# Kernel tuning notes

Hardware: AMD Instinct MI355X
Metric: run time of the kernel (lower is better)

Reference implementation:

```python
import jax, jax.numpy as jnp
import numpy as np

N, FR, P, B = 8192, 128, 4194304, 64
LH1, LH2 = 128, 64

def _mlp(x, W1, b1, W2, b2, W3, b3):
    h = jnp.tanh(x @ W1 + b1)
    h = jnp.tanh(h @ W2 + b2)
    return h @ W3 + b3  # [N, 1]

def setup_inputs() -> dict:
    key = jax.random.key(0)
    ks = jax.random.split(key, 12)
    r = jax.random.normal(ks[0], (N, FR), jnp.float32)
    xyz = jax.random.uniform(ks[1], (N, 3), jnp.float32) * 60.0  # box so distances >> sigma
    p0 = jax.random.randint(ks[2], (P,), 0, N)
    off = jax.random.randint(ks[3], (P,), 1, N)  # avoid self-pairs (D2=0)
    pairs = jnp.stack([p0, (p0 + off) % N], axis=1).astype(jnp.int32)
    num_pairs = jnp.full((B,), P // B, dtype=jnp.int32)
    def lin(k, fin, fout):
        return (jax.random.normal(k, (fin, fout), jnp.float32) / np.sqrt(fin)).astype(jnp.float32)
    sW1, sW2, sW3 = lin(ks[4], FR, LH1), lin(ks[5], LH1, LH2), lin(ks[6], LH2, 1)
    eW1, eW2, eW3 = lin(ks[7], FR, LH1), lin(ks[8], LH1, LH2), lin(ks[9], LH2, 1)
    z1, z2, z3 = jnp.zeros((LH1,), jnp.float32), jnp.zeros((LH2,), jnp.float32), jnp.zeros((1,), jnp.float32)
    return dict(r=r, xyz=xyz, pairs=pairs, num_pairs=num_pairs,
                sW1=sW1, sb1=z1, sW2=sW2, sb2=z2, sW3=sW3, sb3=z3,
                eW1=eW1, eb1=z1, eW2=eW2, eb2=z2, eW3=eW3, eb3=z3)

def reference(r, xyz, pairs, num_pairs, sW1, sb1, sW2, sb2, sW3, sb3,
              eW1, eb1, eW2, eb2, eW3, eb3):
    # D2 gathered at pairs == squared distance between the two atoms of each pair
    dx = xyz[pairs[:, 1]] - xyz[pairs[:, 0]]          # [P, 3]
    D2 = jnp.sum(dx * dx, axis=1, keepdims=True)       # [P, 1]
    inv_D = D2 ** -0.5
    sigma = 4.0 + 10.0 * _mlp(r, sW1, sb1, sW2, sb2, sW3, sb3) ** 2   # [N, 1]
    epsilon = 0.1 * _mlp(r, eW1, eb1, eW2, eb2, eW3, eb3) ** 2        # [N, 1]
    sigma_mixed = jnp.sqrt(sigma[pairs[:, 0]] * sigma[pairs[:, 1]])    # [P, 1]
    epsilon_mixed = jnp.sqrt(epsilon[pairs[:, 0]] * epsilon[pairs[:, 1]])
    s = sigma_mixed * inv_D
    s6 = s ** 6
    E_pair = 4.0 * epsilon_mixed * (s6 * s6 - s6)       # [P, 1]
    seg = jnp.repeat(jnp.arange(B), num_pairs, total_repeat_length=P)
    E = jax.ops.segment_sum(E_pair, seg, num_segments=B)  # [B, 1]
    return E
```

## Files before the change

kernel.cpp:

```cpp
#include <hip/hip_runtime.h>
#include <hip/hip_fp16.h>

#define NATOM 8192
#define FR    128
#define NSEG  64
#define PB    256
#define PT    1024
#define PPT   16

typedef _Float16 v8h __attribute__((ext_vector_type(8)));
typedef _Float16 v4h __attribute__((ext_vector_type(4)));
typedef float    v4f __attribute__((ext_vector_type(4)));

__device__ __forceinline__ float fast_tanh(float x)
{
    float t = __expf(2.f * x);
    return 1.f - 2.f * __builtin_amdgcn_rcpf(t + 1.f);
}

__global__ __launch_bounds__(512) void k_mm(
    const float* __restrict__ r, const float* __restrict__ xyz,
    const float* __restrict__ w1s, const float* __restrict__ b1s,
    const float* __restrict__ w2s, const float* __restrict__ b2s,
    const float* __restrict__ w3s, const float* __restrict__ b3s,
    const float* __restrict__ w1e, const float* __restrict__ b1e,
    const float* __restrict__ w2e, const float* __restrict__ b2e,
    const float* __restrict__ w3e, const float* __restrict__ b3e,
    float4* __restrict__ atomd)
{
    extern __shared__ char ldsraw[];
    _Float16* Wh  = (_Float16*)ldsraw;
    _Float16* Wl  = Wh + 32768;
    _Float16* h1h = Wh;
    _Float16* h1l = Wh + 16384;
    _Float16* W2h = Wh + 32768;
    _Float16* W2l = Wh + 49152;
    float*    mArr = (float*)(ldsraw + 131072);

    const int tid = threadIdx.x;
    const int a0  = blockIdx.x * 64;
    const int l = tid & 63, wv = tid >> 6;
    const int row16 = l & 15, kgrp = l >> 4;
    const int at = wv & 3, chf = wv >> 2;

#pragma unroll
    for (int i = 0; i < 8; ++i) {
        int g = i * 512 + tid;
        int c = g & 255, ch = g >> 8;
        const float* wp = (c < 128) ? (w1s + c) : (w1e + (c - 128));
        v8h hh, ll;
#pragma unroll
        for (int j = 0; j < 8; ++j) {
            float x = wp[(ch * 8 + j) * 128];
            _Float16 h = (_Float16)x;
            hh[j] = h;
            ll[j] = (_Float16)((x - (float)h) * 4096.f);
        }
        int sw = c * 16 + (ch ^ (c & 15));
        *(v8h*)(Wh + sw * 8) = hh;
        *(v8h*)(Wl + sw * 8) = ll;
    }

    v8h rh[4], rl[4];
    {
        const float* rb = r + (size_t)(a0 + at * 16 + row16) * FR + kgrp * 8;
#pragma unroll
        for (int ks = 0; ks < 4; ++ks) {
            float4 x0 = *(const float4*)(rb + ks * 32);
            float4 x1 = *(const float4*)(rb + ks * 32 + 4);
            float xs[8] = {x0.x, x0.y, x0.z, x0.w, x1.x, x1.y, x1.z, x1.w};
#pragma unroll
            for (int j = 0; j < 8; ++j) {
                _Float16 h = (_Float16)xs[j];
                rh[ks][j] = h;
                rl[ks][j] = (_Float16)((xs[j] - (float)h) * 4096.f);
            }
        }
    }
    __syncthreads();

    v4h hpack[8], lpack[8];
#pragma unroll
    for (int ct = 0; ct < 8; ++ct) {
        int crow = chf * 128 + ct * 16 + row16;
        v4f a = {0.f, 0.f, 0.f, 0.f}, cr = {0.f, 0.f, 0.f, 0.f};
        int rbo = crow * 128, sw = crow & 15;
#pragma unroll
        for (int ks = 0; ks < 4; ++ks) {
            int off = rbo + (((ks * 4 + kgrp) ^ sw) * 8);
            v8h wh = *(const v8h*)(Wh + off);
            v8h wl = *(const v8h*)(Wl + off);
            a  = __builtin_amdgcn_mfma_f32_16x16x32_f16(wh, rh[ks], a,  0, 0, 0);
            cr = __builtin_amdgcn_mfma_f32_16x16x32_f16(wh, rl[ks], cr, 0, 0, 0);
            cr = __builtin_amdgcn_mfma_f32_16x16x32_f16(wl, rh[ks], cr, 0, 0, 0);
        }
        int colb = chf * 128 + ct * 16 + kgrp * 4;
        const float* bp = (colb < 128) ? (b1s + colb) : (b1e + (colb - 128));
        float4 bv = *(const float4*)bp;
        float bvx[4] = {bv.x, bv.y, bv.z, bv.w};
#pragma unroll
        for (int j = 0; j < 4; ++j) {
            float v = fast_tanh(a[j] + cr[j] * 2.44140625e-4f + bvx[j]);
            _Float16 h = (_Float16)v;
            hpack[ct][j] = h;
            lpack[ct][j] = (_Float16)((v - (float)h) * 4096.f);
        }
    }
    __syncthreads();

    {
        int arow = at * 16 + row16;
#pragma unroll
        for (int ct = 0; ct < 8; ++ct) {
            int colb = chf * 128 + ct * 16 + kgrp * 4;
            int chs = (colb >> 3) ^ row16;
            int off = arow * 256 + chs * 8 + (colb & 7);
            *(v4h*)(h1h + off) = hpack[ct];
            *(v4h*)(h1l + off) = lpack[ct];
        }
#pragma unroll
        for (int i = 0; i < 4; ++i) {
            int g = i * 512 + tid;
            int c = g & 127, ch = g >> 7;
            const float* wp = (c < 64) ? (w2s + c) : (w2e + (c - 64));
            v8h hh, ll;
#pragma unroll
            for (int j = 0; j < 8; ++j) {
                float x = wp[(ch * 8 + j) * 64];
                _Float16 h = (_Float16)x;
                hh[j] = h;
                ll[j] = (_Float16)((x - (float)h) * 4096.f);
            }
            int sw = c * 16 + (ch ^ (c & 15));
            *(v8h*)(W2h + sw * 8) = hh;
            *(v8h*)(W2l + sw * 8) = ll;
        }
    }
    __syncthreads();

    {
        const int arow = at * 16 + row16;
        v8h bh[4], bl[4];
#pragma unroll
        for (int ks = 0; ks < 4; ++ks) {
            int chunk = chf * 16 + ks * 4 + kgrp;
            int off = arow * 256 + ((chunk ^ row16) * 8);
            bh[ks] = *(const v8h*)(h1h + off);
            bl[ks] = *(const v8h*)(h1l + off);
        }
        float ps = 0.f;
#pragma unroll
        for (int ct2 = 0; ct2 < 4; ++ct2) {
            int c2 = chf * 64 + ct2 * 16 + row16;
            v4f a = {0.f, 0.f, 0.f, 0.f}, cr = {0.f, 0.f, 0.f, 0.f};
            int rbo = c2 * 128, sw = c2 & 15;
#pragma unroll
            for (int ks = 0; ks < 4; ++ks) {
                int off = rbo + (((ks * 4 + kgrp) ^ sw) * 8);
                v8h wh = *(const v8h*)(W2h + off);
                v8h wl = *(const v8h*)(W2l + off);
                a  = __builtin_amdgcn_mfma_f32_16x16x32_f16(wh, bh[ks], a,  0, 0, 0);
                cr = __builtin_amdgcn_mfma_f32_16x16x32_f16(wh, bl[ks], cr, 0, 0, 0);
                cr = __builtin_amdgcn_mfma_f32_16x16x32_f16(wl, bh[ks], cr, 0, 0, 0);
            }
            int cb = ct2 * 16 + kgrp * 4;
            float4 b2v = *(const float4*)((chf ? b2e : b2s) + cb);
            float4 w3v = *(const float4*)((chf ? w3e : w3s) + cb);
            float b2x[4] = {b2v.x, b2v.y, b2v.z, b2v.w};
            float w3x[4] = {w3v.x, w3v.y, w3v.z, w3v.w};
#pragma unroll
            for (int j = 0; j < 4; ++j) {
                float h2 = fast_tanh(a[j] + cr[j] * 2.44140625e-4f + b2x[j]);
                ps = fmaf(h2, w3x[j], ps);
            }
        }
        ps += __shfl_xor(ps, 16);
        ps += __shfl_xor(ps, 32);
        if (l < 16) mArr[chf * 64 + at * 16 + l] = ps + (chf ? b3e[0] : b3s[0]);
    }
    __syncthreads();

    if (tid < 64) {
        int atom = a0 + tid;
        float ms = mArr[tid], me = mArr[64 + tid];
        float sg = fmaf(10.f * ms, ms, 4.f);
        float p  = sg * sqrtf(sg);
        float q  = 0.31622776601683794f * fabsf(me);
        __half2 pq = __halves2half2(__float2half(p), __float2half(q));
        atomd[atom] = make_float4(xyz[3 * atom], xyz[3 * atom + 1],
                                  xyz[3 * atom + 2], __builtin_bit_cast(float, pq));
    }
}

__device__ __forceinline__ float pair_e(const float4* atomd, int ia, int ib)
{
    float4 A = atomd[ia], B = atomd[ib];
    float dx = A.x - B.x, dy = A.y - B.y, dz = A.z - B.z;
    float D2 = fmaf(dx, dx, fmaf(dy, dy, dz * dz));
    float inv = __builtin_amdgcn_rcpf(D2);
    float inv3 = inv * inv * inv;
    __half2 ha = __builtin_bit_cast(__half2, A.w);
    __half2 hb = __builtin_bit_cast(__half2, B.w);
    float pp = __low2float(ha) * __low2float(hb);
    float qq = __high2float(ha) * __high2float(hb);
    float s6 = pp * pp * inv3;
    return 4.f * qq * (s6 * s6 - s6);
}

__global__ __launch_bounds__(PT, 1) void k_pair(
    const float4* __restrict__ atomg, const int* __restrict__ pairs,
    const int* __restrict__ num_pairs,
    float* __restrict__ out, int P)
{
    extern __shared__ char smem[];
    float4* atomd = (float4*)smem;
    int*    off   = (int*)(smem + NATOM * 16);
    float*  bsum  = (float*)(smem + NATOM * 16 + 68 * 4);

    const int tid = threadIdx.x;

#pragma unroll
    for (int i = 0; i < NATOM / PT; ++i) atomd[i * PT + tid] = atomg[i * PT + tid];
    if (tid < 64) {
        int run = num_pairs[tid];
#pragma unroll
        for (int d = 1; d < 64; d <<= 1) {
            int o = __shfl_up(run, d);
            if (tid >= d) run += o;
        }
        off[tid + 1] = run;
        if (tid == 0) off[0] = 0;
        bsum[tid] = 0.f;
    }
    __syncthreads();

    const int base = (blockIdx.x * PT + tid) * PPT;
    const bool fast = (base + PPT <= P);

    if (__all(fast)) {
        int pr2[PPT * 2];
        const int4* pp4 = (const int4*)(pairs + (size_t)base * 2);
#pragma unroll
        for (int i = 0; i < PPT / 2; ++i) {
            int4 v = pp4[i];
            pr2[4*i] = v.x; pr2[4*i+1] = v.y; pr2[4*i+2] = v.z; pr2[4*i+3] = v.w;
        }
        int s = 0;
#pragma unroll
        for (int st = 32; st; st >>= 1) { int ns = s + st; if (ns <= NSEG - 1 && off[ns] <= base) s = ns; }
        float acc = 0.f;
        if (base + PPT <= off[s + 1] || s == NSEG - 1) {
#pragma unroll
            for (int i = 0; i < PPT; ++i)
                acc += pair_e(atomd, pr2[2 * i], pr2[2 * i + 1]);
        } else {
            int off_next = off[s + 1];
#pragma unroll
            for (int i = 0; i < PPT; ++i) {
                int idx = base + i;
                while (s < NSEG - 1 && idx >= off_next) {
                    if (acc != 0.f) atomicAdd(&bsum[s], acc);
                    acc = 0.f; ++s; off_next = off[s + 1];
                }
                acc += pair_e(atomd, pr2[2 * i], pr2[2 * i + 1]);
            }
        }
        int s0 = __builtin_amdgcn_readfirstlane(s);
        if (__all(s == s0)) {
            float v = acc;
#pragma unroll
            for (int o = 32; o; o >>= 1) v += __shfl_xor(v, o);
            if ((tid & 63) == 0) atomicAdd(&bsum[s0], v);
        } else {
            atomicAdd(&bsum[s], acc);
        }
    } else if (base < P) {
        int s = 0;
#pragma unroll
        for (int st = 32; st; st >>= 1) { int ns = s + st; if (ns <= NSEG - 1 && off[ns] <= base) s = ns; }
        int off_next = off[s + 1];
        float acc = 0.f;
        for (int i = 0; i < PPT; ++i) {
            int idx = base + i;
            if (idx >= P) break;
            while (s < NSEG - 1 && idx >= off_next) {
                if (acc != 0.f) atomicAdd(&bsum[s], acc);
                acc = 0.f; ++s; off_next = off[s + 1];
            }
            acc += pair_e(atomd, pairs[2 * (size_t)idx], pairs[2 * (size_t)idx + 1]);
        }
        if (acc != 0.f) atomicAdd(&bsum[s], acc);
    }
    __syncthreads();
    if (tid < NSEG) atomicAdd(&out[tid], bsum[tid]);
}

extern "C" void kernel_launch(void* const* d_in, const int* in_sizes, int n_in,
                              void* d_out, int out_size, void* d_ws, size_t ws_size,
                              hipStream_t stream)
{
    const float* r    = (const float*)d_in[0];
    const float* xyz  = (const float*)d_in[1];
    const int*   prs  = (const int*)d_in[2];
    const int*   np   = (const int*)d_in[3];
    const float* sW1  = (const float*)d_in[4];
    const float* sb1  = (const float*)d_in[5];
    const float* sW2  = (const float*)d_in[6];
    const float* sb2  = (const float*)d_in[7];
    const float* sW3  = (const float*)d_in[8];
    const float* sb3  = (const float*)d_in[9];
    const float* eW1  = (const float*)d_in[10];
    const float* eb1  = (const float*)d_in[11];
    const float* eW2  = (const float*)d_in[12];
    const float* eb2  = (const float*)d_in[13];
    const float* eW3  = (const float*)d_in[14];
    const float* eb3  = (const float*)d_in[15];
    float* out = (float*)d_out;
    const int P = in_sizes[2] / 2;

    float4* atomd = (float4*)d_ws;

    hipMemsetAsync(out, 0, (size_t)out_size * sizeof(float), stream);

    size_t smem1 = 131072 + 512;
    hipFuncSetAttribute((const void*)k_mm, hipFuncAttributeMaxDynamicSharedMemorySize, (int)smem1);
    k_mm<<<NATOM / 64, 512, smem1, stream>>>(r, xyz, sW1, sb1, sW2, sb2, sW3, sb3,
                                             eW1, eb1, eW2, eb2, eW3, eb3, atomd);

    size_t smem = (size_t)NATOM * 16 + 68 * 4 + NSEG * 4;
    hipFuncSetAttribute((const void*)k_pair, hipFuncAttributeMaxDynamicSharedMemorySize, (int)smem);
    k_pair<<<PB, PT, smem, stream>>>(atomd, prs, np, out, P);
}
```

Baseline: 34.79 us.

## Fuse MLP and pair-energy kernels into one launch with inter-block flag sync

Merges the per-atom MLP kernel and the pair-energy reduction kernel into a single 256-block kernel. The first 128 blocks run the MLP on 512 threads and publish per-atom data to global memory. They then release an agent-scope flag that every block spin-waits on before staging the atom table into LDS and reducing pair energies. Idle threads prefetch pair indices while the MLP runs, and the output memset is folded into block 0. This removes a kernel launch, the memset, and the gap between stages. In exchange it requires all blocks to be co-resident, and the flags are never reset, so repeated calls may skip the wait and race with stale workspace data and the output zeroing.

```diff
diff --git a/kernel.cpp b/kernel.cpp
--- a/kernel.cpp
+++ b/kernel.cpp
@@ -4,9 +4,11 @@
 #define NATOM 8192
 #define FR    128
 #define NSEG  64
-#define PB    256
+#define NPROD 128
+#define NBLK  256
 #define PT    1024
 #define PPT   16
+#define SENT  0x5EED1234
 
 typedef _Float16 v8h __attribute__((ext_vector_type(8)));
 typedef _Float16 v4h __attribute__((ext_vector_type(4)));
@@ -16,180 +18,6 @@
 {
     float t = __expf(2.f * x);
     return 1.f - 2.f * __builtin_amdgcn_rcpf(t + 1.f);
-}
-
-__global__ __launch_bounds__(512) void k_mm(
-    const float* __restrict__ r, const float* __restrict__ xyz,
-    const float* __restrict__ w1s, const float* __restrict__ b1s,
-    const float* __restrict__ w2s, const float* __restrict__ b2s,
-    const float* __restrict__ w3s, const float* __restrict__ b3s,
-    const float* __restrict__ w1e, const float* __restrict__ b1e,
-    const float* __restrict__ w2e, const float* __restrict__ b2e,
-    const float* __restrict__ w3e, const float* __restrict__ b3e,
-    float4* __restrict__ atomd)
-{
-    extern __shared__ char ldsraw[];
-    _Float16* Wh  = (_Float16*)ldsraw;
-    _Float16* Wl  = Wh + 32768;
-    _Float16* h1h = Wh;
-    _Float16* h1l = Wh + 16384;
-    _Float16* W2h = Wh + 32768;
-    _Float16* W2l = Wh + 49152;
-    float*    mArr = (float*)(ldsraw + 131072);
-
-    const int tid = threadIdx.x;
-    const int a0  = blockIdx.x * 64;
-    const int l = tid & 63, wv = tid >> 6;
-    const int row16 = l & 15, kgrp = l >> 4;
-    const int at = wv & 3, chf = wv >> 2;
-
-#pragma unroll
-    for (int i = 0; i < 8; ++i) {
-        int g = i * 512 + tid;
-        int c = g & 255, ch = g >> 8;
-        const float* wp = (c < 128) ? (w1s + c) : (w1e + (c - 128));
-        v8h hh, ll;
-#pragma unroll
-        for (int j = 0; j < 8; ++j) {
-            float x = wp[(ch * 8 + j) * 128];
-            _Float16 h = (_Float16)x;
-            hh[j] = h;
-            ll[j] = (_Float16)((x - (float)h) * 4096.f);
-        }
-        int sw = c * 16 + (ch ^ (c & 15));
-        *(v8h*)(Wh + sw * 8) = hh;
-        *(v8h*)(Wl + sw * 8) = ll;
-    }
-
-    v8h rh[4], rl[4];
-    {
-        const float* rb = r + (size_t)(a0 + at * 16 + row16) * FR + kgrp * 8;
-#pragma unroll
-        for (int ks = 0; ks < 4; ++ks) {
-            float4 x0 = *(const float4*)(rb + ks * 32);
-            float4 x1 = *(const float4*)(rb + ks * 32 + 4);
-            float xs[8] = {x0.x, x0.y, x0.z, x0.w, x1.x, x1.y, x1.z, x1.w};
-#pragma unroll
-            for (int j = 0; j < 8; ++j) {
-                _Float16 h = (_Float16)xs[j];
-                rh[ks][j] = h;
-                rl[ks][j] = (_Float16)((xs[j] - (float)h) * 4096.f);
-            }
-        }
-    }
-    __syncthreads();
-
-    v4h hpack[8], lpack[8];
-#pragma unroll
-    for (int ct = 0; ct < 8; ++ct) {
-        int crow = chf * 128 + ct * 16 + row16;
-        v4f a = {0.f, 0.f, 0.f, 0.f}, cr = {0.f, 0.f, 0.f, 0.f};
-        int rbo = crow * 128, sw = crow & 15;
-#pragma unroll
-        for (int ks = 0; ks < 4; ++ks) {
-            int off = rbo + (((ks * 4 + kgrp) ^ sw) * 8);
-            v8h wh = *(const v8h*)(Wh + off);
-            v8h wl = *(const v8h*)(Wl + off);
-            a  = __builtin_amdgcn_mfma_f32_16x16x32_f16(wh, rh[ks], a,  0, 0, 0);
-            cr = __builtin_amdgcn_mfma_f32_16x16x32_f16(wh, rl[ks], cr, 0, 0, 0);
-            cr = __builtin_amdgcn_mfma_f32_16x16x32_f16(wl, rh[ks], cr, 0, 0, 0);
-        }
-        int colb = chf * 128 + ct * 16 + kgrp * 4;
-        const float* bp = (colb < 128) ? (b1s + colb) : (b1e + (colb - 128));
-        float4 bv = *(const float4*)bp;
-        float bvx[4] = {bv.x, bv.y, bv.z, bv.w};
-#pragma unroll
-        for (int j = 0; j < 4; ++j) {
-            float v = fast_tanh(a[j] + cr[j] * 2.44140625e-4f + bvx[j]);
-            _Float16 h = (_Float16)v;
-            hpack[ct][j] = h;
-            lpack[ct][j] = (_Float16)((v - (float)h) * 4096.f);
-        }
-    }
-    __syncthreads();
-
-    {
-        int arow = at * 16 + row16;
-#pragma unroll
-        for (int ct = 0; ct < 8; ++ct) {
-            int colb = chf * 128 + ct * 16 + kgrp * 4;
-            int chs = (colb >> 3) ^ row16;
-            int off = arow * 256 + chs * 8 + (colb & 7);
-            *(v4h*)(h1h + off) = hpack[ct];
-            *(v4h*)(h1l + off) = lpack[ct];
-        }
-#pragma unroll
-        for (int i = 0; i < 4; ++i) {
-            int g = i * 512 + tid;
-            int c = g & 127, ch = g >> 7;
-            const float* wp = (c < 64) ? (w2s + c) : (w2e + (c - 64));
-            v8h hh, ll;
-#pragma unroll
-            for (int j = 0; j < 8; ++j) {
-                float x = wp[(ch * 8 + j) * 64];
-                _Float16 h = (_Float16)x;
-                hh[j] = h;
-                ll[j] = (_Float16)((x - (float)h) * 4096.f);
-            }
-            int sw = c * 16 + (ch ^ (c & 15));
-            *(v8h*)(W2h + sw * 8) = hh;
-            *(v8h*)(W2l + sw * 8) = ll;
-        }
-    }
-    __syncthreads();
-
-    {
-        const int arow = at * 16 + row16;
-        v8h bh[4], bl[4];
-#pragma unroll
-        for (int ks = 0; ks < 4; ++ks) {
-            int chunk = chf * 16 + ks * 4 + kgrp;
-            int off = arow * 256 + ((chunk ^ row16) * 8);
-            bh[ks] = *(const v8h*)(h1h + off);
-            bl[ks] = *(const v8h*)(h1l + off);
-        }
-        float ps = 0.f;
-#pragma unroll
-        for (int ct2 = 0; ct2 < 4; ++ct2) {
-            int c2 = chf * 64 + ct2 * 16 + row16;
-            v4f a = {0.f, 0.f, 0.f, 0.f}, cr = {0.f, 0.f, 0.f, 0.f};
-            int rbo = c2 * 128, sw = c2 & 15;
-#pragma unroll
-            for (int ks = 0; ks < 4; ++ks) {
-                int off = rbo + (((ks * 4 + kgrp) ^ sw) * 8);
-                v8h wh = *(const v8h*)(W2h + off);
-                v8h wl = *(const v8h*)(W2l + off);
-                a  = __builtin_amdgcn_mfma_f32_16x16x32_f16(wh, bh[ks], a,  0, 0, 0);
-                cr = __builtin_amdgcn_mfma_f32_16x16x32_f16(wh, bl[ks], cr, 0, 0, 0);
-                cr = __builtin_amdgcn_mfma_f32_16x16x32_f16(wl, bh[ks], cr, 0, 0, 0);
-            }
-            int cb = ct2 * 16 + kgrp * 4;
-            float4 b2v = *(const float4*)((chf ? b2e : b2s) + cb);
-            float4 w3v = *(const float4*)((chf ? w3e : w3s) + cb);
-            float b2x[4] = {b2v.x, b2v.y, b2v.z, b2v.w};
-            float w3x[4] = {w3v.x, w3v.y, w3v.z, w3v.w};
-#pragma unroll
-            for (int j = 0; j < 4; ++j) {
-                float h2 = fast_tanh(a[j] + cr[j] * 2.44140625e-4f + b2x[j]);
-                ps = fmaf(h2, w3x[j], ps);
-            }
-        }
-        ps += __shfl_xor(ps, 16);
-        ps += __shfl_xor(ps, 32);
-        if (l < 16) mArr[chf * 64 + at * 16 + l] = ps + (chf ? b3e[0] : b3s[0]);
-    }
-    __syncthreads();
-
-    if (tid < 64) {
-        int atom = a0 + tid;
-        float ms = mArr[tid], me = mArr[64 + tid];
-        float sg = fmaf(10.f * ms, ms, 4.f);
-        float p  = sg * sqrtf(sg);
-        float q  = 0.31622776601683794f * fabsf(me);
-        __half2 pq = __halves2half2(__float2half(p), __float2half(q));
-        atomd[atom] = make_float4(xyz[3 * atom], xyz[3 * atom + 1],
-                                  xyz[3 * atom + 2], __builtin_bit_cast(float, pq));
-    }
 }
 
 __device__ __forceinline__ float pair_e(const float4* atomd, int ia, int ib)
@@ -207,92 +35,293 @@
     return 4.f * qq * (s6 * s6 - s6);
 }
 
-__global__ __launch_bounds__(PT, 1) void k_pair(
-    const float4* __restrict__ atomg, const int* __restrict__ pairs,
-    const int* __restrict__ num_pairs,
+__global__ __launch_bounds__(PT, 4) void k_fused(
+    const float* __restrict__ r, const float* __restrict__ xyz,
+    const int* __restrict__ pairs, const int* __restrict__ num_pairs,
+    const float* __restrict__ w1s, const float* __restrict__ b1s,
+    const float* __restrict__ w2s, const float* __restrict__ b2s,
+    const float* __restrict__ w3s, const float* __restrict__ b3s,
+    const float* __restrict__ w1e, const float* __restrict__ b1e,
+    const float* __restrict__ w2e, const float* __restrict__ b2e,
+    const float* __restrict__ w3e, const float* __restrict__ b3e,
+    float4* __restrict__ atomd, int* __restrict__ flags,
     float* __restrict__ out, int P)
 {
-    extern __shared__ char smem[];
-    float4* atomd = (float4*)smem;
-    int*    off   = (int*)(smem + NATOM * 16);
-    float*  bsum  = (float*)(smem + NATOM * 16 + 68 * 4);
-
+    extern __shared__ char ldsraw[];
     const int tid = threadIdx.x;
-
-#pragma unroll
-    for (int i = 0; i < NATOM / PT; ++i) atomd[i * PT + tid] = atomg[i * PT + tid];
-    if (tid < 64) {
-        int run = num_pairs[tid];
-#pragma unroll
-        for (int d = 1; d < 64; d <<= 1) {
-            int o = __shfl_up(run, d);
-            if (tid >= d) run += o;
-        }
-        off[tid + 1] = run;
-        if (tid == 0) off[0] = 0;
-        bsum[tid] = 0.f;
-    }
-    __syncthreads();
-
-    const int base = (blockIdx.x * PT + tid) * PPT;
+    const int bid = blockIdx.x;
+    const bool prod = (bid < NPROD);
+
+    if (bid == 0 && tid < NSEG) out[tid] = 0.f;
+
+    const int base = (bid * PT + tid) * PPT;
     const bool fast = (base + PPT <= P);
-
-    if (__all(fast)) {
-        int pr2[PPT * 2];
+    int pr2[PPT * 2];
+
+    if ((!prod || tid >= 512) && fast) {
         const int4* pp4 = (const int4*)(pairs + (size_t)base * 2);
 #pragma unroll
         for (int i = 0; i < PPT / 2; ++i) {
             int4 v = pp4[i];
             pr2[4*i] = v.x; pr2[4*i+1] = v.y; pr2[4*i+2] = v.z; pr2[4*i+3] = v.w;
         }
-        int s = 0;
-#pragma unroll
-        for (int st = 32; st; st >>= 1) { int ns = s + st; if (ns <= NSEG - 1 && off[ns] <= base) s = ns; }
-        float acc = 0.f;
-        if (base + PPT <= off[s + 1] || s == NSEG - 1) {
-#pragma unroll
-            for (int i = 0; i < PPT; ++i)
-                acc += pair_e(atomd, pr2[2 * i], pr2[2 * i + 1]);
-        } else {
+    }
+
+    {
+        _Float16* Wh  = (_Float16*)ldsraw;
+        _Float16* Wl  = Wh + 32768;
+        _Float16* h1h = Wh;
+        _Float16* h1l = Wh + 16384;
+        _Float16* W2h = Wh + 32768;
+        _Float16* W2l = Wh + 49152;
+        float*    mArr = (float*)(ldsraw + 131072);
+
+        const int a0  = bid * 64;
+        const int l = tid & 63, wv = tid >> 6;
+        const int row16 = l & 15, kgrp = l >> 4;
+        const int at = wv & 3, chf = wv >> 2;
+        const bool mlp = prod && (tid < 512);
+
+        v8h rh[4], rl[4];
+        if (mlp) {
+#pragma unroll
+            for (int i = 0; i < 8; ++i) {
+                int g = i * 512 + tid;
+                int c = g & 255, ch = g >> 8;
+                const float* wp = (c < 128) ? (w1s + c) : (w1e + (c - 128));
+                v8h hh, ll;
+#pragma unroll
+                for (int j = 0; j < 8; ++j) {
+                    float x = wp[(ch * 8 + j) * 128];
+                    _Float16 h = (_Float16)x;
+                    hh[j] = h;
+                    ll[j] = (_Float16)((x - (float)h) * 4096.f);
+                }
+                int sw = c * 16 + (ch ^ (c & 15));
+                *(v8h*)(Wh + sw * 8) = hh;
+                *(v8h*)(Wl + sw * 8) = ll;
+            }
+            const float* rb = r + (size_t)(a0 + at * 16 + row16) * FR + kgrp * 8;
+#pragma unroll
+            for (int ks = 0; ks < 4; ++ks) {
+                float4 x0 = *(const float4*)(rb + ks * 32);
+                float4 x1 = *(const float4*)(rb + ks * 32 + 4);
+                float xs[8] = {x0.x, x0.y, x0.z, x0.w, x1.x, x1.y, x1.z, x1.w};
+#pragma unroll
+                for (int j = 0; j < 8; ++j) {
+                    _Float16 h = (_Float16)xs[j];
+                    rh[ks][j] = h;
+                    rl[ks][j] = (_Float16)((xs[j] - (float)h) * 4096.f);
+                }
+            }
+        }
+        __syncthreads();
+
+        v4h hpack[8], lpack[8];
+        if (mlp) {
+#pragma unroll
+            for (int ct = 0; ct < 8; ++ct) {
+                int crow = chf * 128 + ct * 16 + row16;
+                v4f a = {0.f, 0.f, 0.f, 0.f}, cr = {0.f, 0.f, 0.f, 0.f};
+                int rbo = crow * 128, sw = crow & 15;
+#pragma unroll
+                for (int ks = 0; ks < 4; ++ks) {
+                    int off = rbo + (((ks * 4 + kgrp) ^ sw) * 8);
+                    v8h wh = *(const v8h*)(Wh + off);
+                    v8h wl = *(const v8h*)(Wl + off);
+                    a  = __builtin_amdgcn_mfma_f32_16x16x32_f16(wh, rh[ks], a,  0, 0, 0);
+                    cr = __builtin_amdgcn_mfma_f32_16x16x32_f16(wh, rl[ks], cr, 0, 0, 0);
+                    cr = __builtin_amdgcn_mfma_f32_16x16x32_f16(wl, rh[ks], cr, 0, 0, 0);
+                }
+                int colb = chf * 128 + ct * 16 + kgrp * 4;
+                const float* bp = (colb < 128) ? (b1s + colb) : (b1e + (colb - 128));
+                float4 bv = *(const float4*)bp;
+                float bvx[4] = {bv.x, bv.y, bv.z, bv.w};
+#pragma unroll
+                for (int j = 0; j < 4; ++j) {
+                    float v = fast_tanh(a[j] + cr[j] * 2.44140625e-4f + bvx[j]);
+                    _Float16 h = (_Float16)v;
+                    hpack[ct][j] = h;
+                    lpack[ct][j] = (_Float16)((v - (float)h) * 4096.f);
+                }
+            }
+        }
+        __syncthreads();
+
+        if (mlp) {
+            int arow = at * 16 + row16;
+#pragma unroll
+            for (int ct = 0; ct < 8; ++ct) {
+                int colb = chf * 128 + ct * 16 + kgrp * 4;
+                int chs = (colb >> 3) ^ row16;
+                int off = arow * 256 + chs * 8 + (colb & 7);
+                *(v4h*)(h1h + off) = hpack[ct];
+                *(v4h*)(h1l + off) = lpack[ct];
+            }
+#pragma unroll
+            for (int i = 0; i < 4; ++i) {
+                int g = i * 512 + tid;
+                int c = g & 127, ch = g >> 7;
+                const float* wp = (c < 64) ? (w2s + c) : (w2e + (c - 64));
+                v8h hh, ll;
+#pragma unroll
+                for (int j = 0; j < 8; ++j) {
+                    float x = wp[(ch * 8 + j) * 64];
+                    _Float16 h = (_Float16)x;
+                    hh[j] = h;
+                    ll[j] = (_Float16)((x - (float)h) * 4096.f);
+                }
+                int sw = c * 16 + (ch ^ (c & 15));
+                *(v8h*)(W2h + sw * 8) = hh;
+                *(v8h*)(W2l + sw * 8) = ll;
+            }
+        }
+        __syncthreads();
+
+        if (mlp) {
+            const int arow = at * 16 + row16;
+            v8h bh[4], bl[4];
+#pragma unroll
+            for (int ks = 0; ks < 4; ++ks) {
+                int chunk = chf * 16 + ks * 4 + kgrp;
+                int off = arow * 256 + ((chunk ^ row16) * 8);
+                bh[ks] = *(const v8h*)(h1h + off);
+                bl[ks] = *(const v8h*)(h1l + off);
+            }
+            float ps = 0.f;
+#pragma unroll
+            for (int ct2 = 0; ct2 < 4; ++ct2) {
+                int c2 = chf * 64 + ct2 * 16 + row16;
+                v4f a = {0.f, 0.f, 0.f, 0.f}, cr = {0.f, 0.f, 0.f, 0.f};
+                int rbo = c2 * 128, sw = c2 & 15;
+#pragma unroll
+                for (int ks = 0; ks < 4; ++ks) {
+                    int off = rbo + (((ks * 4 + kgrp) ^ sw) * 8);
+                    v8h wh = *(const v8h*)(W2h + off);
+                    v8h wl = *(const v8h*)(W2l + off);
+                    a  = __builtin_amdgcn_mfma_f32_16x16x32_f16(wh, bh[ks], a,  0, 0, 0);
+                    cr = __builtin_amdgcn_mfma_f32_16x16x32_f16(wh, bl[ks], cr, 0, 0, 0);
+                    cr = __builtin_amdgcn_mfma_f32_16x16x32_f16(wl, bh[ks], cr, 0, 0, 0);
+                }
+                int cb = ct2 * 16 + kgrp * 4;
+                float4 b2v = *(const float4*)((chf ? b2e : b2s) + cb);
+                float4 w3v = *(const float4*)((chf ? w3e : w3s) + cb);
+                float b2x[4] = {b2v.x, b2v.y, b2v.z, b2v.w};
+                float w3x[4] = {w3v.x, w3v.y, w3v.z, w3v.w};
+#pragma unroll
+                for (int j = 0; j < 4; ++j) {
+                    float h2 = fast_tanh(a[j] + cr[j] * 2.44140625e-4f + b2x[j]);
+                    ps = fmaf(h2, w3x[j], ps);
+                }
+            }
+            ps += __shfl_xor(ps, 16);
+            ps += __shfl_xor(ps, 32);
+            if (l < 16) mArr[chf * 64 + at * 16 + l] = ps + (chf ? b3e[0] : b3s[0]);
+        }
+        __syncthreads();
+
+        if (prod && tid < 64) {
+            int atom = a0 + tid;
+            float ms = mArr[tid], me = mArr[64 + tid];
+            float sg = fmaf(10.f * ms, ms, 4.f);
+            float p  = sg * sqrtf(sg);
+            float q  = 0.31622776601683794f * fabsf(me);
+            __half2 pq = __halves2half2(__float2half(p), __float2half(q));
+            atomd[atom] = make_float4(xyz[3 * atom], xyz[3 * atom + 1],
+                                      xyz[3 * atom + 2], __builtin_bit_cast(float, pq));
+        }
+        __syncthreads();
+        if (prod && tid == 0) {
+            __threadfence();
+            __hip_atomic_store(&flags[bid], SENT, __ATOMIC_RELEASE, __HIP_MEMORY_SCOPE_AGENT);
+        }
+    }
+
+    if (prod && tid < 512 && fast) {
+        const int4* pp4 = (const int4*)(pairs + (size_t)base * 2);
+#pragma unroll
+        for (int i = 0; i < PPT / 2; ++i) {
+            int4 v = pp4[i];
+            pr2[4*i] = v.x; pr2[4*i+1] = v.y; pr2[4*i+2] = v.z; pr2[4*i+3] = v.w;
+        }
+    }
+
+    if (tid < NPROD) {
+        while (__hip_atomic_load(&flags[tid], __ATOMIC_ACQUIRE, __HIP_MEMORY_SCOPE_AGENT) != SENT)
+            __builtin_amdgcn_s_sleep(8);
+    }
+    __syncthreads();
+
+    {
+        float4* atomdL = (float4*)ldsraw;
+        int*    off    = (int*)(ldsraw + 131072);
+        float*  bsum   = (float*)(ldsraw + 131072 + 272);
+
+#pragma unroll
+        for (int i = 0; i < NATOM / PT; ++i) atomdL[i * PT + tid] = atomd[i * PT + tid];
+        if (tid < 64) {
+            int run = num_pairs[tid];
+#pragma unroll
+            for (int d = 1; d < 64; d <<= 1) {
+                int o = __shfl_up(run, d);
+                if (tid >= d) run += o;
+            }
+            off[tid + 1] = run;
+            if (tid == 0) off[0] = 0;
+            bsum[tid] = 0.f;
+        }
+        __syncthreads();
+
+        if (__all(fast)) {
+            int s = 0;
+#pragma unroll
+            for (int st = 32; st; st >>= 1) { int ns = s + st; if (ns <= NSEG - 1 && off[ns] <= base) s = ns; }
+            float acc = 0.f;
+            if (base + PPT <= off[s + 1] || s == NSEG - 1) {
+#pragma unroll
+                for (int i = 0; i < PPT; ++i)
+                    acc += pair_e(atomdL, pr2[2 * i], pr2[2 * i + 1]);
+            } else {
+                int off_next = off[s + 1];
+#pragma unroll
+                for (int i = 0; i < PPT; ++i) {
+                    int idx = base + i;
+                    while (s < NSEG - 1 && idx >= off_next) {
+                        if (acc != 0.f) atomicAdd(&bsum[s], acc);
+                        acc = 0.f; ++s; off_next = off[s + 1];
+                    }
+                    acc += pair_e(atomdL, pr2[2 * i], pr2[2 * i + 1]);
+                }
+            }
+            int s0 = __builtin_amdgcn_readfirstlane(s);
+            if (__all(s == s0)) {
+                float v = acc;
+#pragma unroll
+                for (int o = 32; o; o >>= 1) v += __shfl_xor(v, o);
+                if ((tid & 63) == 0) atomicAdd(&bsum[s0], v);
+            } else {
+                atomicAdd(&bsum[s], acc);
+            }
+        } else if (base < P) {
+            int s = 0;
+#pragma unroll
+            for (int st = 32; st; st >>= 1) { int ns = s + st; if (ns <= NSEG - 1 && off[ns] <= base) s = ns; }
             int off_next = off[s + 1];
-#pragma unroll
+            float acc = 0.f;
             for (int i = 0; i < PPT; ++i) {
                 int idx = base + i;
+                if (idx >= P) break;
                 while (s < NSEG - 1 && idx >= off_next) {
                     if (acc != 0.f) atomicAdd(&bsum[s], acc);
                     acc = 0.f; ++s; off_next = off[s + 1];
                 }
-                acc += pair_e(atomd, pr2[2 * i], pr2[2 * i + 1]);
-            }
-        }
-        int s0 = __builtin_amdgcn_readfirstlane(s);
-        if (__all(s == s0)) {
-            float v = acc;
-#pragma unroll
-            for (int o = 32; o; o >>= 1) v += __shfl_xor(v, o);
-            if ((tid & 63) == 0) atomicAdd(&bsum[s0], v);
-        } else {
-            atomicAdd(&bsum[s], acc);
-        }
-    } else if (base < P) {
-        int s = 0;
-#pragma unroll
-        for (int st = 32; st; st >>= 1) { int ns = s + st; if (ns <= NSEG - 1 && off[ns] <= base) s = ns; }
-        int off_next = off[s + 1];
-        float acc = 0.f;
-        for (int i = 0; i < PPT; ++i) {
-            int idx = base + i;
-            if (idx >= P) break;
-            while (s < NSEG - 1 && idx >= off_next) {
-                if (acc != 0.f) atomicAdd(&bsum[s], acc);
-                acc = 0.f; ++s; off_next = off[s + 1];
-            }
-            acc += pair_e(atomd, pairs[2 * (size_t)idx], pairs[2 * (size_t)idx + 1]);
-        }
-        if (acc != 0.f) atomicAdd(&bsum[s], acc);
-    }
-    __syncthreads();
-    if (tid < NSEG) atomicAdd(&out[tid], bsum[tid]);
+                acc += pair_e(atomdL, pairs[2 * (size_t)idx], pairs[2 * (size_t)idx + 1]);
+            }
+            if (acc != 0.f) atomicAdd(&bsum[s], acc);
+        }
+        __syncthreads();
+        if (tid < NSEG) atomicAdd(&out[tid], bsum[tid]);
+    }
 }
 
 extern "C" void kernel_launch(void* const* d_in, const int* in_sizes, int n_in,
@@ -319,15 +348,12 @@
     const int P = in_sizes[2] / 2;
 
     float4* atomd = (float4*)d_ws;
-
-    hipMemsetAsync(out, 0, (size_t)out_size * sizeof(float), stream);
-
-    size_t smem1 = 131072 + 512;
-    hipFuncSetAttribute((const void*)k_mm, hipFuncAttributeMaxDynamicSharedMemorySize, (int)smem1);
-    k_mm<<<NATOM / 64, 512, smem1, stream>>>(r, xyz, sW1, sb1, sW2, sb2, sW3, sb3,
-                                             eW1, eb1, eW2, eb2, eW3, eb3, atomd);
-
-    size_t smem = (size_t)NATOM * 16 + 68 * 4 + NSEG * 4;
-    hipFuncSetAttribute((const void*)k_pair, hipFuncAttributeMaxDynamicSharedMemorySize, (int)smem);
-    k_pair<<<PB, PT, smem, stream>>>(atomd, prs, np, out, P);
+    int*    flags = (int*)((char*)d_ws + 131072);
+
+    size_t smem = 131072 + 272 + 256;
+    hipFuncSetAttribute((const void*)k_fused, hipFuncAttributeMaxDynamicSharedMemorySize, (int)smem);
+    k_fused<<<NBLK, PT, smem, stream>>>(r, xyz, prs, np,
+                                        sW1, sb1, sW2, sb2, sW3, sb3,
+                                        eW1, eb1, eW2, eb2, eW3, eb3,
+                                        atomd, flags, out, P);
 }
```

Measured after the change: 40.22 us. +15.6%, slower.
